# Kernel optimization log

Measured on AMD Instinct MI355X. Metric: run time of the kernel, lower is better.

The kernel has to match this reference:

```python
import jax, jax.numpy as jnp
import numpy as np

EPS = 1e-5

def layernorm(x, g, b):
    mu = jnp.mean(x, axis=-1, keepdims=True)
    var = jnp.mean((x - mu) ** 2, axis=-1, keepdims=True)
    return (x - mu) * jax.lax.rsqrt(var + EPS) * g + b

def cswin_attn(q, k, v, lepe_w, lepe_b, H, W, H_sp, W_sp, num_heads):
    # q,k,v: (B, L, C) with C = branch dim
    B, L, C = q.shape
    d = C // num_heads
    nH, nW = H // H_sp, W // W_sp
    def to_win(t):
        t = t.transpose(0, 2, 1).reshape(B, C, nH, H_sp, nW, W_sp)
        t = t.transpose(0, 2, 4, 3, 5, 1).reshape(B * nH * nW, H_sp * W_sp, num_heads, d)
        return t.transpose(0, 2, 1, 3)  # (Bw, h, N, d)
    kw = to_win(k)
    vw = to_win(v)
    # q windows as images for LePE depthwise conv
    qi = q.transpose(0, 2, 1).reshape(B, C, nH, H_sp, nW, W_sp)
    qi = qi.transpose(0, 2, 4, 1, 3, 5).reshape(B * nH * nW, C, H_sp, W_sp)
    lepe = jax.lax.conv_general_dilated(qi, lepe_w, (1, 1), 'SAME',
                                        feature_group_count=C,
                                        dimension_numbers=('NCHW', 'OIHW', 'NCHW'))
    lepe = lepe + lepe_b[None, :, None, None]
    lepe = lepe.reshape(-1, num_heads, d, H_sp * W_sp).transpose(0, 1, 3, 2)
    qw = qi.reshape(-1, num_heads, d, H_sp * W_sp).transpose(0, 1, 3, 2) * (float(d) ** -0.5)
    attn = jax.nn.softmax(jnp.einsum('whnd,whmd->whnm', qw, kw), axis=-1)
    out = jnp.einsum('whnm,whmd->whnd', attn, vw) + lepe  # (Bw, h, N, d)
    out = out.transpose(0, 2, 1, 3).reshape(B, nH, nW, H_sp, W_sp, C)
    out = out.transpose(0, 1, 3, 2, 4, 5).reshape(B, H * W, C)
    return out

def setup_inputs() -> dict:
    key = jax.random.key(0)
    ks = jax.random.split(key, 20)
    B, C, H, W = 8, 128, 64, 64
    ch_z = 512
    hid = 4 * C
    Cb = C // 2  # branch dim
    s = lambda fin: (1.0 / np.sqrt(fin))
    inp = {
        'x': jax.random.normal(ks[0], (B, C, H, W), jnp.float32),
        'z': jax.random.normal(ks[1], (B, ch_z), jnp.float32),
        'ln1_g': jnp.ones((C,), jnp.float32), 'ln1_b': jnp.zeros((C,), jnp.float32),
        'ln2_g': jnp.ones((C,), jnp.float32), 'ln2_b': jnp.zeros((C,), jnp.float32),
        'Wz1': jax.random.normal(ks[2], (C, ch_z), jnp.float32) * s(ch_z),
        'Wz2': jax.random.normal(ks[3], (C, ch_z), jnp.float32) * s(ch_z),
        'Wqkv': jax.random.normal(ks[4], (3 * C, C), jnp.float32) * s(C),
        'Wproj': jax.random.normal(ks[5], (C, C), jnp.float32) * s(C),
        'bproj': jnp.zeros((C,), jnp.float32),
        'lepe_w0': jax.random.normal(ks[6], (Cb, 1, 3, 3), jnp.float32) * (1.0 / 3.0),
        'lepe_b0': jnp.zeros((Cb,), jnp.float32),
        'lepe_w1': jax.random.normal(ks[7], (Cb, 1, 3, 3), jnp.float32) * (1.0 / 3.0),
        'lepe_b1': jnp.zeros((Cb,), jnp.float32),
        'W1': jax.random.normal(ks[8], (hid, C), jnp.float32) * s(C),
        'b1': jnp.zeros((hid,), jnp.float32),
        'W2': jax.random.normal(ks[9], (C, hid), jnp.float32) * s(hid),
        'b2': jnp.zeros((C,), jnp.float32),
    }
    return inp

def reference(x, z, ln1_g, ln1_b, ln2_g, ln2_b, Wz1, Wz2, Wqkv, Wproj, bproj,
              lepe_w0, lepe_b0, lepe_w1, lepe_b1, W1, b1, W2, b2):
    B, C, H, W = x.shape
    nh = 4  # num_heads // 2 per branch
    ss = 8  # split_size
    Cb = C // 2
    xf = x.reshape(B, C, H * W).transpose(0, 2, 1)  # (B, L, C)
    # code-conditioned attention branch
    z1 = z @ Wz1.T  # (B, C)
    h1 = layernorm(xf, ln1_g, ln1_b) + z1[:, None, :]
    qkv = (h1 @ Wqkv.T).reshape(B, H * W, 3, C).transpose(2, 0, 1, 3)  # (3, B, L, C)
    q, k, v = qkv[0], qkv[1], qkv[2]
    x1 = cswin_attn(q[..., :Cb], k[..., :Cb], v[..., :Cb], lepe_w0, lepe_b0, H, W, H, ss, nh)
    x2 = cswin_attn(q[..., Cb:], k[..., Cb:], v[..., Cb:], lepe_w1, lepe_b1, H, W, ss, W, nh)
    att = jnp.concatenate([x1, x2], axis=2) @ Wproj.T + bproj
    xf = xf + att
    # code-conditioned MLP branch
    z2 = z @ Wz2.T
    h2 = layernorm(xf, ln2_g, ln2_b) + z2[:, None, :]
    mlp = jax.nn.gelu(h2 @ W1.T + b1, approximate=False) @ W2.T + b2
    xf = xf + mlp
    return xf.transpose(0, 2, 1).reshape(B, C, H, W)
```

## Files before the change

### kernel.cpp

```cpp
#include <hip/hip_runtime.h>
#include <cstddef>

__device__ __forceinline__ float b2f(unsigned short u) {
  return __uint_as_float(((unsigned int)u) << 16);
}
__device__ __forceinline__ unsigned short f2b(float f) {
  unsigned int u = __float_as_uint(f);
  u = u + 0x7FFFu + ((u >> 16) & 1u);
  return (unsigned short)(u >> 16);
}
__device__ __forceinline__ unsigned int pk2(float lo, float hi) {
  unsigned int ulo = __float_as_uint(lo) + 0x8000u;
  unsigned int uhi = __float_as_uint(hi) + 0x8000u;
  return __builtin_amdgcn_perm(uhi, ulo, 0x07060302u);
}
__device__ __forceinline__ float gelu_exact(float x) {
  return 0.5f * x * (1.0f + erff(x * 0.70710678118654752f));
}

#if defined(__has_builtin)
#if __has_builtin(__builtin_amdgcn_exp2f)
#define EXP2(x) __builtin_amdgcn_exp2f(x)
#else
#define EXP2(x) __expf((x) * 0.6931471805599453f)
#endif
#else
#define EXP2(x) __expf((x) * 0.6931471805599453f)
#endif

typedef __attribute__((ext_vector_type(8))) short bf16x8;
typedef __attribute__((ext_vector_type(4))) float f32x4;

__global__ void k_detect(const unsigned short* __restrict__ g,
                         unsigned int* __restrict__ flag) {
  if (threadIdx.x == 0 && blockIdx.x == 0) *flag = (g[0] == 0x3F80u) ? 1u : 0u;
}

struct Ptrs18 { const void* p[18]; };
__constant__ const int c_off[19] = {
    0, 4096, 4224, 4352, 4480, 4608, 70144, 135680, 184832, 201216,
    201344, 201920, 201984, 202560, 202624, 268160, 268672, 334208, 334336};

__global__ __launch_bounds__(256) void k_convert(Ptrs18 ptrs,
                                                 const unsigned int* __restrict__ flagp,
                                                 unsigned short* __restrict__ dst) {
  int idx = blockIdx.x * 256 + threadIdx.x;
  if (idx >= 334336) return;
  unsigned int flag = *flagp;
  int i = 0;
#pragma unroll
  for (int t = 1; t < 18; ++t) i += (idx >= c_off[t]);
  int local = idx - c_off[i];
  if (flag) dst[idx] = ((const unsigned short*)ptrs.p[i])[local];
  else      dst[idx] = f2b(((const float*)ptrs.p[i])[local]);
}

__global__ __launch_bounds__(256) void k_transpose_in(const void* __restrict__ x,
                                                      const unsigned int* __restrict__ flagp,
                                                      float* __restrict__ xf) {
  __shared__ float t[32][33];
  unsigned int flag = *flagp;
  int b = blockIdx.z;
  int l0 = blockIdx.x * 32, c0 = blockIdx.y * 32;
  int tx = threadIdx.x & 31, ty = threadIdx.x >> 5;
#pragma unroll
  for (int i = 0; i < 32; i += 8) {
    size_t gi = ((size_t)b * 128 + c0 + ty + i) * 4096 + l0 + tx;
    t[ty + i][tx] = flag ? b2f(((const unsigned short*)x)[gi]) : ((const float*)x)[gi];
  }
  __syncthreads();
#pragma unroll
  for (int i = 0; i < 32; i += 8)
    xf[((size_t)b * 4096 + l0 + ty + i) * 128 + c0 + tx] = t[tx][ty + i];
}

__global__ __launch_bounds__(256) void k_transpose_out(const float* __restrict__ xf,
                                                       const unsigned int* __restrict__ flagp,
                                                       void* __restrict__ out) {
  __shared__ float t[32][33];
  unsigned int flag = *flagp;
  int b = blockIdx.z;
  int l0 = blockIdx.x * 32, c0 = blockIdx.y * 32;
  int tx = threadIdx.x & 31, ty = threadIdx.x >> 5;
#pragma unroll
  for (int i = 0; i < 32; i += 8)
    t[ty + i][tx] = xf[((size_t)b * 4096 + l0 + ty + i) * 128 + c0 + tx];
  __syncthreads();
#pragma unroll
  for (int i = 0; i < 32; i += 8) {
    size_t gi = ((size_t)b * 128 + c0 + ty + i) * 4096 + l0 + tx;
    float v = t[tx][ty + i];
    if (flag) ((unsigned short*)out)[gi] = f2b(v);
    else      ((float*)out)[gi] = v;
  }
}

__global__ __launch_bounds__(256) void k_zmm(const unsigned short* __restrict__ z,
                                             const unsigned short* __restrict__ Wz1,
                                             const unsigned short* __restrict__ Wz2,
                                             float* __restrict__ zz) {
  __shared__ float sz[512];
  int b = blockIdx.x, tid = threadIdx.x;
  sz[tid]       = b2f(z[b * 512 + tid]);
  sz[tid + 256] = b2f(z[b * 512 + 256 + tid]);
  __syncthreads();
  const unsigned short* W = (tid < 128) ? Wz1 : Wz2;
  int c = tid & 127;
  const unsigned short* wr = W + c * 512;
  float acc = 0.f;
  for (int k = 0; k < 512; k += 4) {
    ushort4 wv = *(const ushort4*)&wr[k];
    acc += b2f(wv.x) * sz[k] + b2f(wv.y) * sz[k + 1] + b2f(wv.z) * sz[k + 2] + b2f(wv.w) * sz[k + 3];
  }
  zz[b * 256 + tid] = acc;
}

__global__ __launch_bounds__(256) void k_ln(const float* __restrict__ x,
                                            const unsigned short* __restrict__ g,
                                            const unsigned short* __restrict__ bb,
                                            const float* __restrict__ zz, int zsel,
                                            unsigned short* __restrict__ out) {
  int row = blockIdx.x * 4 + (threadIdx.x >> 6);
  int lane = threadIdx.x & 63;
  int b = row >> 12;
  const float* xr = x + (size_t)row * 128;
  float2 v = *(const float2*)&xr[lane * 2];
  float s = v.x + v.y, s2 = v.x * v.x + v.y * v.y;
#pragma unroll
  for (int m = 32; m; m >>= 1) {
    s += __shfl_xor(s, m, 64);
    s2 += __shfl_xor(s2, m, 64);
  }
  float mu = s * 0.0078125f;
  float var = s2 * 0.0078125f - mu * mu;
  float rstd = rsqrtf(var + 1e-5f);
  int c = lane * 2;
  const float* zr = zz + b * 256 + zsel * 128;
  float ox = (v.x - mu) * rstd * b2f(g[c])     + b2f(bb[c])     + zr[c];
  float oy = (v.y - mu) * rstd * b2f(g[c + 1]) + b2f(bb[c + 1]) + zr[c + 1];
  ushort2 o2; o2.x = f2b(ox); o2.y = f2b(oy);
  *(ushort2*)&out[(size_t)row * 128 + c] = o2;
}

__global__ __launch_bounds__(256) void k_gemm_mfma(const unsigned short* __restrict__ A,
                                                   const unsigned short* __restrict__ W,
                                                   const unsigned short* __restrict__ bias,
                                                   const float* __restrict__ res,
                                                   void* __restrict__ out,
                                                   int M, int N, int K, int ldw, int flags) {
  __shared__ unsigned short As[128][40];
  __shared__ unsigned short Ws[128][40];
  int bm = blockIdx.x * 128, bn = blockIdx.y * 128;
  int tid = threadIdx.x;
  int lane = tid & 63, wv = tid >> 6;
  int wm = (wv >> 1) * 64, wn = (wv & 1) * 64;
  int qd = lane >> 4, l15 = lane & 15;
  f32x4 acc[4][4] = {};
  for (int k0 = 0; k0 < K; k0 += 32) {
    __syncthreads();
#pragma unroll
    for (int i = tid; i < 512; i += 256) {
      int row = i >> 2, c8 = (i & 3) << 3;
      *(bf16x8*)&As[row][c8] = *(const bf16x8*)&A[(size_t)(bm + row) * K + k0 + c8];
      *(bf16x8*)&Ws[row][c8] = *(const bf16x8*)&W[(size_t)(bn + row) * ldw + k0 + c8];
    }
    __syncthreads();
    bf16x8 af[4], bfr[4];
#pragma unroll
    for (int t = 0; t < 4; ++t) {
      af[t]  = *(const bf16x8*)&As[wm + t * 16 + l15][qd * 8];
      bfr[t] = *(const bf16x8*)&Ws[wn + t * 16 + l15][qd * 8];
    }
#pragma unroll
    for (int mi = 0; mi < 4; ++mi)
#pragma unroll
      for (int nj = 0; nj < 4; ++nj)
        acc[mi][nj] = __builtin_amdgcn_mfma_f32_16x16x32_bf16(af[mi], bfr[nj],
                                                              acc[mi][nj], 0, 0, 0);
  }
  if (flags & 4) {
#pragma unroll
    for (int mi = 0; mi < 4; ++mi)
#pragma unroll
      for (int r = 0; r < 4; ++r) {
        int row = bm + wm + mi * 16 + qd * 4 + r;
        int bb2 = row >> 12, l = row & 4095;
        int hI = l >> 6, wI = l & 63;
        int s0 = wI >> 3, t0 = hI * 8 + (wI & 7);
        int s1 = hI >> 3, t1 = (hI & 7) * 64 + wI;
#pragma unroll
        for (int nj = 0; nj < 4; ++nj) {
          int colb = bn + wn + nj * 16;
          int kv = colb >> 7, br = (colb >> 6) & 1, hh2 = (colb >> 4) & 3;
          int ss = br ? s1 : s0, tt = br ? t1 : t0;
          size_t addr = ((((size_t)((kv * 8 + bb2) * 2 + br) * 4 + hh2) * 8 + ss) * 512 + tt) * 16 + l15;
          ((unsigned short*)out)[addr] = f2b(acc[mi][nj][r]);
        }
      }
    return;
  }
  float bv[4];
#pragma unroll
  for (int nj = 0; nj < 4; ++nj)
    bv[nj] = bias ? b2f(bias[bn + wn + nj * 16 + l15]) : 0.f;
#pragma unroll
  for (int mi = 0; mi < 4; ++mi) {
#pragma unroll
    for (int r = 0; r < 4; ++r) {
      int row = bm + wm + mi * 16 + qd * 4 + r;
#pragma unroll
      for (int nj = 0; nj < 4; ++nj) {
        int col = bn + wn + nj * 16 + l15;
        float t = acc[mi][nj][r] + bv[nj];
        if (flags & 1) t = gelu_exact(t);
        if (res) t += res[(size_t)row * N + col];
        if (flags & 2) ((unsigned short*)out)[(size_t)row * N + col] = f2b(t);
        else           ((float*)out)[(size_t)row * N + col] = t;
      }
    }
  }
}

__global__ __launch_bounds__(256) void k_gemm64(const unsigned short* __restrict__ A,
                                                const unsigned short* __restrict__ W,
                                                const unsigned short* __restrict__ bias,
                                                const float* __restrict__ res,
                                                void* __restrict__ out,
                                                int M, int N, int K, int ldw, int flags) {
  __shared__ unsigned short As[64][40];
  __shared__ unsigned short Ws[128][40];
  int bm = blockIdx.x * 64, bn = blockIdx.y * 128;
  int tid = threadIdx.x;
  int lane = tid & 63, wv = tid >> 6;
  int qd = lane >> 4, l15 = lane & 15;
  f32x4 acc[4][2] = {};
  for (int k0 = 0; k0 < K; k0 += 32) {
    __syncthreads();
    {
      int row = tid >> 2, c8 = (tid & 3) << 3;
      *(bf16x8*)&As[row][c8] = *(const bf16x8*)&A[(size_t)(bm + row) * K + k0 + c8];
    }
#pragma unroll
    for (int i = tid; i < 512; i += 256) {
      int row = i >> 2, c8 = (i & 3) << 3;
      *(bf16x8*)&Ws[row][c8] = *(const bf16x8*)&W[(size_t)(bn + row) * ldw + k0 + c8];
    }
    __syncthreads();
    bf16x8 af[4], bfr[2];
#pragma unroll
    for (int t = 0; t < 4; ++t) af[t] = *(const bf16x8*)&As[t * 16 + l15][qd * 8];
#pragma unroll
    for (int t = 0; t < 2; ++t) bfr[t] = *(const bf16x8*)&Ws[wv * 32 + t * 16 + l15][qd * 8];
#pragma unroll
    for (int mi = 0; mi < 4; ++mi)
#pragma unroll
      for (int nj = 0; nj < 2; ++nj)
        acc[mi][nj] = __builtin_amdgcn_mfma_f32_16x16x32_bf16(af[mi], bfr[nj],
                                                              acc[mi][nj], 0, 0, 0);
  }
  float bv[2];
#pragma unroll
  for (int nj = 0; nj < 2; ++nj)
    bv[nj] = bias ? b2f(bias[bn + wv * 32 + nj * 16 + l15]) : 0.f;
#pragma unroll
  for (int mi = 0; mi < 4; ++mi) {
#pragma unroll
    for (int r = 0; r < 4; ++r) {
      int row = bm + mi * 16 + qd * 4 + r;
#pragma unroll
      for (int nj = 0; nj < 2; ++nj) {
        int col = bn + wv * 32 + nj * 16 + l15;
        float t = acc[mi][nj][r] + bv[nj];
        if (flags & 1) t = gelu_exact(t);
        if (res) t += res[(size_t)row * N + col];
        if (flags & 2) ((unsigned short*)out)[(size_t)row * N + col] = f2b(t);
        else           ((float*)out)[(size_t)row * N + col] = t;
      }
    }
  }
}

__global__ __launch_bounds__(256, 3) void k_mlp(float* __restrict__ xf,
                                                const unsigned short* __restrict__ g,
                                                const unsigned short* __restrict__ bb,
                                                const float* __restrict__ zz,
                                                const unsigned short* __restrict__ W1,
                                                const unsigned short* __restrict__ b1,
                                                const unsigned short* __restrict__ W2,
                                                const unsigned short* __restrict__ b2) {
  __shared__ unsigned short As_all[64][136];
  __shared__ unsigned short Ws[128][40];
  __shared__ unsigned short Hs[4][64][40];
  int tid = threadIdx.x;
  int bm = blockIdx.x * 64;
  int bidx = bm >> 12;
  {
    int row = tid >> 2, part = tid & 3;
    const float* xr = xf + ((size_t)(bm + row) * 128 + part * 32);
    float v[32];
#pragma unroll
    for (int i = 0; i < 8; ++i) *(float4*)&v[i * 4] = *(const float4*)&xr[i * 4];
    float s = 0.f, s2 = 0.f;
#pragma unroll
    for (int i = 0; i < 32; ++i) { s += v[i]; s2 += v[i] * v[i]; }
    s  += __shfl_xor(s, 1, 64);  s  += __shfl_xor(s, 2, 64);
    s2 += __shfl_xor(s2, 1, 64); s2 += __shfl_xor(s2, 2, 64);
    float mu = s * 0.0078125f;
    float var = s2 * 0.0078125f - mu * mu;
    float rstd = rsqrtf(var + 1e-5f);
    const float* zr = zz + bidx * 256 + 128 + part * 32;
#pragma unroll
    for (int i = 0; i < 32; i += 2) {
      int c = part * 32 + i;
      float ox = (v[i]     - mu) * rstd * b2f(g[c])     + b2f(bb[c])     + zr[i];
      float oy = (v[i + 1] - mu) * rstd * b2f(g[c + 1]) + b2f(bb[c + 1]) + zr[i + 1];
      unsigned int u = (unsigned int)f2b(ox) | ((unsigned int)f2b(oy) << 16);
      *(unsigned int*)&As_all[row][c] = u;
    }
  }
  int lane = tid & 63, wv = tid >> 6;
  int qd = lane >> 4, l15 = lane & 15;
  f32x4 acc2[4][2] = {};
#pragma unroll 1
  for (int j = 0; j < 4; ++j) {
    f32x4 acc1[4][2] = {};
    const unsigned short* W1j = W1 + j * 128 * 128;
#pragma unroll 1
    for (int ks = 0; ks < 4; ++ks) {
      __syncthreads();
#pragma unroll
      for (int i = tid; i < 512; i += 256) {
        int rw = i >> 2, c8 = (i & 3) << 3;
        *(bf16x8*)&Ws[rw][c8] = *(const bf16x8*)&W1j[rw * 128 + ks * 32 + c8];
      }
      __syncthreads();
      bf16x8 af[4], bfr[2];
#pragma unroll
      for (int t = 0; t < 4; ++t)
        af[t] = *(const bf16x8*)&As_all[t * 16 + l15][qd * 8 + ks * 32];
#pragma unroll
      for (int t = 0; t < 2; ++t)
        bfr[t] = *(const bf16x8*)&Ws[wv * 32 + t * 16 + l15][qd * 8];
#pragma unroll
      for (int mi = 0; mi < 4; ++mi)
#pragma unroll
        for (int nj = 0; nj < 2; ++nj)
          acc1[mi][nj] = __builtin_amdgcn_mfma_f32_16x16x32_bf16(af[mi], bfr[nj],
                                                                 acc1[mi][nj], 0, 0, 0);
    }
    float bv1[2];
#pragma unroll
    for (int nj = 0; nj < 2; ++nj)
      bv1[nj] = b2f(b1[j * 128 + wv * 32 + nj * 16 + l15]);
#pragma unroll
    for (int mi = 0; mi < 4; ++mi)
#pragma unroll
      for (int nj = 0; nj < 2; ++nj)
#pragma unroll
        for (int r = 0; r < 4; ++r) {
          float t = gelu_exact(acc1[mi][nj][r] + bv1[nj]);
          Hs[wv][mi * 16 + qd * 4 + r][nj * 16 + l15] = f2b(t);
        }
#pragma unroll 1
    for (int ks = 0; ks < 4; ++ks) {
      __syncthreads();
#pragma unroll
      for (int i = tid; i < 512; i += 256) {
        int rw = i >> 2, c8 = (i & 3) << 3;
        *(bf16x8*)&Ws[rw][c8] = *(const bf16x8*)&W2[rw * 512 + j * 128 + ks * 32 + c8];
      }
      __syncthreads();
      bf16x8 af2[4], bfr2[2];
#pragma unroll
      for (int t = 0; t < 4; ++t)
        af2[t] = *(const bf16x8*)&Hs[ks][t * 16 + l15][qd * 8];
#pragma unroll
      for (int t = 0; t < 2; ++t)
        bfr2[t] = *(const bf16x8*)&Ws[wv * 32 + t * 16 + l15][qd * 8];
#pragma unroll
      for (int mi = 0; mi < 4; ++mi)
#pragma unroll
        for (int nj = 0; nj < 2; ++nj)
          acc2[mi][nj] = __builtin_amdgcn_mfma_f32_16x16x32_bf16(af2[mi], bfr2[nj],
                                                                 acc2[mi][nj], 0, 0, 0);
    }
  }
  float bv2[2];
#pragma unroll
  for (int nj = 0; nj < 2; ++nj)
    bv2[nj] = b2f(b2[wv * 32 + nj * 16 + l15]);
#pragma unroll
  for (int mi = 0; mi < 4; ++mi)
#pragma unroll
    for (int r = 0; r < 4; ++r) {
      int row = mi * 16 + qd * 4 + r;
#pragma unroll
      for (int nj = 0; nj < 2; ++nj) {
        int col = wv * 32 + nj * 16 + l15;
        size_t gi = (size_t)(bm + row) * 128 + col;
        float t = acc2[mi][nj][r] + bv2[nj] + xf[gi];
        xf[gi] = t;
      }
    }
}

__global__ __launch_bounds__(256, 4) void k_attn_mfma(const unsigned short* __restrict__ qkvw,
                                                      const unsigned short* __restrict__ lw0,
                                                      const unsigned short* __restrict__ lb0,
                                                      const unsigned short* __restrict__ lw1,
                                                      const unsigned short* __restrict__ lb1,
                                                      unsigned short* __restrict__ att) {
  __shared__ unsigned short Ks[512][16];
  __shared__ unsigned short Vt[16][520];
  const size_t S1 = 4194304;
  int branch = blockIdx.y;
  int bx = blockIdx.x;
  int half = bx & 1, wh = bx >> 1;
  int w = wh >> 2, hh = wh & 3;
  int b = w >> 3, s = w & 7;
  int cb = branch * 64 + hh * 16;
  size_t slab = ((size_t)(((b * 2 + branch) * 4 + hh) * 8 + s)) * 8192;
  const unsigned short* Qg = qkvw + slab;
  const unsigned short* Kg = qkvw + S1 + slab;
  const unsigned short* Vg = qkvw + 2 * S1 + slab;
  int tid = threadIdx.x;
  for (int i = tid; i < 1024; i += 256) {
    int tok = i >> 1, c8 = (i & 1) << 3;
    *(bf16x8*)&Ks[tok][c8] = *(const bf16x8*)&Kg[tok * 16 + c8];
    bf16x8 vv = *(const bf16x8*)&Vg[tok * 16 + c8];
    int col = (tok & ~31) | ((tok & 12) << 1) | ((tok & 16) >> 2) | (tok & 3);
#pragma unroll
    for (int j = 0; j < 8; ++j) Vt[c8 + j][col] = (unsigned short)vv[j];
  }
  __syncthreads();
  int lane = tid & 63, wv = tid >> 6;
  int qd = lane >> 4, l15 = lane & 15;
  int koff = (qd & 1) * 8;
  const unsigned short* lwp = branch ? lw1 : lw0;
  const unsigned short* lbp = branch ? lb1 : lb0;
  float wreg[4][9], breg[4];
#pragma unroll
  for (int r = 0; r < 4; ++r) {
    int cc = hh * 16 + qd * 4 + r;
    breg[r] = b2f(lbp[cc]);
#pragma unroll
    for (int j = 0; j < 9; ++j) wreg[r][j] = b2f(lwp[cc * 9 + j]);
  }
  int sy = branch ? 64 : 8;
  int yl = branch ? 8 : 64;
  int xl = branch ? 64 : 8;
  const float QSCALE = 0.25f * 1.44269504f;
  const float NS = -11.5415603f;
  const f32x4 NSHIFT = {NS, NS, NS, NS};
#pragma unroll 1
  for (int qt = 0; qt < 4; ++qt) {
    int q0 = half * 256 + wv * 64 + qt * 16;
    int tq = q0 + l15;
    bf16x8 qf = {};
    if (qd < 2) {
      bf16x8 raw = *(const bf16x8*)&Qg[tq * 16 + qd * 8];
#pragma unroll
      for (int j = 0; j < 8; ++j)
        qf[j] = (short)f2b(b2f((unsigned short)raw[j]) * QSCALE);
    }
    float lsum = 0.f;
    f32x4 O0 = {0.f, 0.f, 0.f, 0.f}, O1 = {0.f, 0.f, 0.f, 0.f};
#pragma unroll 1
    for (int kc = 0; kc < 4; ++kc) {
      f32x4 sc[8];
#pragma unroll
      for (int c = 0; c < 8; ++c) {
        bf16x8 kf = *(const bf16x8*)&Ks[kc * 128 + c * 16 + l15][koff];
        sc[c] = __builtin_amdgcn_mfma_f32_16x16x32_bf16(kf, qf, NSHIFT, 0, 0, 0);
      }
      float csum = 0.f;
#pragma unroll
      for (int c = 0; c < 8; ++c) {
        float e0 = EXP2(sc[c][0]), e1 = EXP2(sc[c][1]);
        float e2 = EXP2(sc[c][2]), e3 = EXP2(sc[c][3]);
        csum += (e0 + e1) + (e2 + e3);
        sc[c][0] = __uint_as_float(pk2(e0, e1));
        sc[c][1] = __uint_as_float(pk2(e2, e3));
      }
      lsum += csum;
#pragma unroll
      for (int bc = 0; bc < 4; ++bc) {
        union { unsigned int u[4]; bf16x8 v; } pu;
        pu.u[0] = __float_as_uint(sc[2 * bc][0]);
        pu.u[1] = __float_as_uint(sc[2 * bc][1]);
        pu.u[2] = __float_as_uint(sc[2 * bc + 1][0]);
        pu.u[3] = __float_as_uint(sc[2 * bc + 1][1]);
        bf16x8 vf = *(const bf16x8*)&Vt[l15][kc * 128 + bc * 32 + qd * 8];
        if (bc & 1) O1 = __builtin_amdgcn_mfma_f32_16x16x32_bf16(vf, pu.v, O1, 0, 0, 0);
        else        O0 = __builtin_amdgcn_mfma_f32_16x16x32_bf16(vf, pu.v, O0, 0, 0, 0);
      }
    }
    lsum += __shfl_xor(lsum, 16, 64);
    lsum += __shfl_xor(lsum, 32, 64);
    int y = branch ? (tq >> 6) : (tq >> 3);
    int x = branch ? (tq & 63) : (tq & 7);
    float lep[4] = {breg[0], breg[1], breg[2], breg[3]};
#pragma unroll
    for (int dy = -1; dy <= 1; ++dy)
#pragma unroll
      for (int dx = -1; dx <= 1; ++dx) {
        if ((unsigned)(y + dy) < (unsigned)yl && (unsigned)(x + dx) < (unsigned)xl) {
          int tn = tq + dy * sy + dx;
          int j = (dy + 1) * 3 + (dx + 1);
          ushort4 qv = *(const ushort4*)&Qg[tn * 16 + qd * 4];
          lep[0] += wreg[0][j] * b2f(qv.x);
          lep[1] += wreg[1][j] * b2f(qv.y);
          lep[2] += wreg[2][j] * b2f(qv.z);
          lep[3] += wreg[3][j] * b2f(qv.w);
        }
      }
    float inv = 1.f / lsum;
    int lo = branch ? (s * 8 + y) * 64 + x : y * 64 + s * 8 + x;
    unsigned short* op = att + ((size_t)(b * 4096 + lo)) * 128 + cb + qd * 4;
    ushort4 o;
    o.x = f2b((O0[0] + O1[0]) * inv + lep[0]);
    o.y = f2b((O0[1] + O1[1]) * inv + lep[1]);
    o.z = f2b((O0[2] + O1[2]) * inv + lep[2]);
    o.w = f2b((O0[3] + O1[3]) * inv + lep[3]);
    *(ushort4*)op = o;
  }
}

extern "C" void kernel_launch(void* const* d_in, const int* in_sizes, int n_in,
                              void* d_out, int out_size, void* d_ws, size_t ws_size,
                              hipStream_t stream) {
  const size_t S = 4194304;
  float* ws = (float*)d_ws;
  unsigned int* flag = (unsigned int*)ws;
  float* zz = ws + 64;
  unsigned short* norm = (unsigned short*)(ws + 2112);
  float* xf = ws + 169472;
  unsigned short* h   = (unsigned short*)(ws + 169472 + S);
  unsigned short* qkv = (unsigned short*)(ws + 169472 + S + S / 2);
  unsigned short* att = h;

  const unsigned short* z     = norm + 0;
  const unsigned short* ln1g  = norm + 4096;
  const unsigned short* ln1b  = norm + 4224;
  const unsigned short* ln2g  = norm + 4352;
  const unsigned short* ln2b  = norm + 4480;
  const unsigned short* Wz1   = norm + 4608;
  const unsigned short* Wz2   = norm + 70144;
  const unsigned short* Wqkv  = norm + 135680;
  const unsigned short* Wproj = norm + 184832;
  const unsigned short* bproj = norm + 201216;
  const unsigned short* lw0   = norm + 201344;
  const unsigned short* lb0   = norm + 201920;
  const unsigned short* lw1   = norm + 201984;
  const unsigned short* lb1   = norm + 202560;
  const unsigned short* W1    = norm + 202624;
  const unsigned short* b1    = norm + 268160;
  const unsigned short* W2    = norm + 268672;
  const unsigned short* b2    = norm + 334208;

  Ptrs18 ptrs;
  for (int i = 0; i < 18; ++i) ptrs.p[i] = d_in[i + 1];

  dim3 t256(256);
  k_detect<<<dim3(1), dim3(64), 0, stream>>>((const unsigned short*)d_in[2], flag);
  k_convert<<<dim3(1306), t256, 0, stream>>>(ptrs, flag, (unsigned short*)norm);
  k_transpose_in<<<dim3(128, 4, 8), t256, 0, stream>>>(d_in[0], flag, xf);
  k_zmm<<<dim3(8), t256, 0, stream>>>(z, Wz1, Wz2, zz);
  k_ln<<<dim3(8192), t256, 0, stream>>>(xf, ln1g, ln1b, zz, 0, h);
  k_gemm_mfma<<<dim3(256, 3), t256, 0, stream>>>(h, Wqkv, nullptr, nullptr, qkv,
                                                 32768, 384, 128, 128, 2 | 4);
  k_attn_mfma<<<dim3(512, 2), t256, 0, stream>>>(qkv, lw0, lb0, lw1, lb1, att);
  k_gemm64<<<dim3(512, 1), t256, 0, stream>>>(att, Wproj, bproj, xf, xf,
                                              32768, 128, 128, 128, 0);
  k_mlp<<<dim3(512), t256, 0, stream>>>(xf, ln2g, ln2b, zz, W1, b1, W2, b2);
  k_transpose_out<<<dim3(128, 4, 8), t256, 0, stream>>>(xf, flag, d_out);
}
```

Baseline: 242.5 us.

## Load weight fragments directly from global memory and stage full-K activations once

The GEMM kernels and the fused MLP kernel stop staging weight tiles in shared memory. Each wave now reads its B fragments straight from global memory (the weights are small and likely cache-resident). The GEMM kernels load the whole K=128 activation slab into LDS once, which removes the per-k-step barriers. The MLP kernel's occupancy hint rises from 3 to 4 blocks, since the weight buffer no longer takes LDS. Risks: the GEMMs now hardcode K=128, and the GELU epilogue option was removed from the 128-tile GEMM, which breaks any caller that relied on it.

```diff
diff --git a/kernel.cpp b/kernel.cpp
--- a/kernel.cpp
+++ b/kernel.cpp
@@ -148,28 +148,26 @@
                                                    const float* __restrict__ res,
                                                    void* __restrict__ out,
                                                    int M, int N, int K, int ldw, int flags) {
-  __shared__ unsigned short As[128][40];
-  __shared__ unsigned short Ws[128][40];
+  __shared__ unsigned short As[128][136];
   int bm = blockIdx.x * 128, bn = blockIdx.y * 128;
   int tid = threadIdx.x;
   int lane = tid & 63, wv = tid >> 6;
   int wm = (wv >> 1) * 64, wn = (wv & 1) * 64;
   int qd = lane >> 4, l15 = lane & 15;
+#pragma unroll
+  for (int i = tid; i < 2048; i += 256) {
+    int row = i >> 4, c8 = (i & 15) << 3;
+    *(bf16x8*)&As[row][c8] = *(const bf16x8*)&A[(size_t)(bm + row) * 128 + c8];
+  }
+  __syncthreads();
   f32x4 acc[4][4] = {};
-  for (int k0 = 0; k0 < K; k0 += 32) {
-    __syncthreads();
-#pragma unroll
-    for (int i = tid; i < 512; i += 256) {
-      int row = i >> 2, c8 = (i & 3) << 3;
-      *(bf16x8*)&As[row][c8] = *(const bf16x8*)&A[(size_t)(bm + row) * K + k0 + c8];
-      *(bf16x8*)&Ws[row][c8] = *(const bf16x8*)&W[(size_t)(bn + row) * ldw + k0 + c8];
-    }
-    __syncthreads();
+#pragma unroll
+  for (int ks = 0; ks < 4; ++ks) {
     bf16x8 af[4], bfr[4];
 #pragma unroll
     for (int t = 0; t < 4; ++t) {
-      af[t]  = *(const bf16x8*)&As[wm + t * 16 + l15][qd * 8];
-      bfr[t] = *(const bf16x8*)&Ws[wn + t * 16 + l15][qd * 8];
+      af[t]  = *(const bf16x8*)&As[wm + t * 16 + l15][ks * 32 + qd * 8];
+      bfr[t] = *(const bf16x8*)&W[(size_t)(bn + wn + t * 16 + l15) * ldw + ks * 32 + qd * 8];
     }
 #pragma unroll
     for (int mi = 0; mi < 4; ++mi)
@@ -212,7 +210,6 @@
       for (int nj = 0; nj < 4; ++nj) {
         int col = bn + wn + nj * 16 + l15;
         float t = acc[mi][nj][r] + bv[nj];
-        if (flags & 1) t = gelu_exact(t);
         if (res) t += res[(size_t)row * N + col];
         if (flags & 2) ((unsigned short*)out)[(size_t)row * N + col] = f2b(t);
         else           ((float*)out)[(size_t)row * N + col] = t;
@@ -227,30 +224,27 @@
                                                 const float* __restrict__ res,
                                                 void* __restrict__ out,
                                                 int M, int N, int K, int ldw, int flags) {
-  __shared__ unsigned short As[64][40];
-  __shared__ unsigned short Ws[128][40];
+  __shared__ unsigned short As[64][136];
   int bm = blockIdx.x * 64, bn = blockIdx.y * 128;
   int tid = threadIdx.x;
   int lane = tid & 63, wv = tid >> 6;
   int qd = lane >> 4, l15 = lane & 15;
+#pragma unroll
+  for (int i = tid; i < 1024; i += 256) {
+    int row = i >> 4, c8 = (i & 15) << 3;
+    *(bf16x8*)&As[row][c8] = *(const bf16x8*)&A[(size_t)(bm + row) * 128 + c8];
+  }
+  __syncthreads();
   f32x4 acc[4][2] = {};
-  for (int k0 = 0; k0 < K; k0 += 32) {
-    __syncthreads();
-    {
-      int row = tid >> 2, c8 = (tid & 3) << 3;
-      *(bf16x8*)&As[row][c8] = *(const bf16x8*)&A[(size_t)(bm + row) * K + k0 + c8];
-    }
-#pragma unroll
-    for (int i = tid; i < 512; i += 256) {
-      int row = i >> 2, c8 = (i & 3) << 3;
-      *(bf16x8*)&Ws[row][c8] = *(const bf16x8*)&W[(size_t)(bn + row) * ldw + k0 + c8];
-    }
-    __syncthreads();
+#pragma unroll
+  for (int ks = 0; ks < 4; ++ks) {
     bf16x8 af[4], bfr[2];
 #pragma unroll
-    for (int t = 0; t < 4; ++t) af[t] = *(const bf16x8*)&As[t * 16 + l15][qd * 8];
-#pragma unroll
-    for (int t = 0; t < 2; ++t) bfr[t] = *(const bf16x8*)&Ws[wv * 32 + t * 16 + l15][qd * 8];
+    for (int t = 0; t < 4; ++t)
+      af[t] = *(const bf16x8*)&As[t * 16 + l15][ks * 32 + qd * 8];
+#pragma unroll
+    for (int t = 0; t < 2; ++t)
+      bfr[t] = *(const bf16x8*)&W[(size_t)(bn + wv * 32 + t * 16 + l15) * ldw + ks * 32 + qd * 8];
 #pragma unroll
     for (int mi = 0; mi < 4; ++mi)
 #pragma unroll
@@ -280,7 +274,7 @@
   }
 }
 
-__global__ __launch_bounds__(256, 3) void k_mlp(float* __restrict__ xf,
+__global__ __launch_bounds__(256, 4) void k_mlp(float* __restrict__ xf,
                                                 const unsigned short* __restrict__ g,
                                                 const unsigned short* __restrict__ bb,
                                                 const float* __restrict__ zz,
@@ -289,7 +283,6 @@
                                                 const unsigned short* __restrict__ W2,
                                                 const unsigned short* __restrict__ b2) {
   __shared__ unsigned short As_all[64][136];
-  __shared__ unsigned short Ws[128][40];
   __shared__ unsigned short Hs[4][64][40];
   int tid = threadIdx.x;
   int bm = blockIdx.x * 64;
@@ -318,6 +311,7 @@
       *(unsigned int*)&As_all[row][c] = u;
     }
   }
+  __syncthreads();
   int lane = tid & 63, wv = tid >> 6;
   int qd = lane >> 4, l15 = lane & 15;
   f32x4 acc2[4][2] = {};
@@ -325,22 +319,15 @@
   for (int j = 0; j < 4; ++j) {
     f32x4 acc1[4][2] = {};
     const unsigned short* W1j = W1 + j * 128 * 128;
-#pragma unroll 1
+#pragma unroll
     for (int ks = 0; ks < 4; ++ks) {
-      __syncthreads();
-#pragma unroll
-      for (int i = tid; i < 512; i += 256) {
-        int rw = i >> 2, c8 = (i & 3) << 3;
-        *(bf16x8*)&Ws[rw][c8] = *(const bf16x8*)&W1j[rw * 128 + ks * 32 + c8];
-      }
-      __syncthreads();
       bf16x8 af[4], bfr[2];
 #pragma unroll
       for (int t = 0; t < 4; ++t)
-        af[t] = *(const bf16x8*)&As_all[t * 16 + l15][qd * 8 + ks * 32];
+        af[t] = *(const bf16x8*)&As_all[t * 16 + l15][ks * 32 + qd * 8];
 #pragma unroll
       for (int t = 0; t < 2; ++t)
-        bfr[t] = *(const bf16x8*)&Ws[wv * 32 + t * 16 + l15][qd * 8];
+        bfr[t] = *(const bf16x8*)&W1j[(wv * 32 + t * 16 + l15) * 128 + ks * 32 + qd * 8];
 #pragma unroll
       for (int mi = 0; mi < 4; ++mi)
 #pragma unroll
@@ -348,6 +335,7 @@
           acc1[mi][nj] = __builtin_amdgcn_mfma_f32_16x16x32_bf16(af[mi], bfr[nj],
                                                                  acc1[mi][nj], 0, 0, 0);
     }
+    if (j) __syncthreads();
     float bv1[2];
 #pragma unroll
     for (int nj = 0; nj < 2; ++nj)
@@ -361,22 +349,16 @@
           float t = gelu_exact(acc1[mi][nj][r] + bv1[nj]);
           Hs[wv][mi * 16 + qd * 4 + r][nj * 16 + l15] = f2b(t);
         }
-#pragma unroll 1
+    __syncthreads();
+#pragma unroll
     for (int ks = 0; ks < 4; ++ks) {
-      __syncthreads();
-#pragma unroll
-      for (int i = tid; i < 512; i += 256) {
-        int rw = i >> 2, c8 = (i & 3) << 3;
-        *(bf16x8*)&Ws[rw][c8] = *(const bf16x8*)&W2[rw * 512 + j * 128 + ks * 32 + c8];
-      }
-      __syncthreads();
       bf16x8 af2[4], bfr2[2];
 #pragma unroll
       for (int t = 0; t < 4; ++t)
         af2[t] = *(const bf16x8*)&Hs[ks][t * 16 + l15][qd * 8];
 #pragma unroll
       for (int t = 0; t < 2; ++t)
-        bfr2[t] = *(const bf16x8*)&Ws[wv * 32 + t * 16 + l15][qd * 8];
+        bfr2[t] = *(const bf16x8*)&W2[(wv * 32 + t * 16 + l15) * 512 + j * 128 + ks * 32 + qd * 8];
 #pragma unroll
       for (int mi = 0; mi < 4; ++mi)
 #pragma unroll
```

Result: faster. 236.5 us (-2.5%).
